# Optimization experiments

Measured on AMD Instinct MI355X. Metric: run time of the kernel, lower is better.

## Reference

```python
import jax, jax.numpy as jnp
import numpy as np

# LightGCN propagation constants
N_USERS = 50000
N_ITEMS = 100000
N_NODES = N_USERS + N_ITEMS          # rows of the symmetric normalized adjacency
N_EDGES = 2400000                    # nnz of sparse adjacency (avg degree ~16)
LATENT_DIM = 64                      # config['latent_dim_rec']
N_LAYERS = 3                         # config['lightGCN_n_layers']
BATCH = 4096


def setup_inputs() -> dict:
    key = jax.random.key(0)
    ks = jax.random.split(key, 7)
    # Embedding tables, init std=0.1 as in nn.init.normal_(std=0.1)
    emb_user = 0.1 * jax.random.normal(ks[0], (N_USERS, LATENT_DIM), dtype=jnp.float32)
    emb_item = 0.1 * jax.random.normal(ks[1], (N_ITEMS, LATENT_DIM), dtype=jnp.float32)
    # Sparse normalized adjacency in COO form (fixed structure reused every layer)
    src = jax.random.randint(ks[2], (N_EDGES,), 0, N_NODES, dtype=jnp.int32)
    dst = jax.random.randint(ks[3], (N_EDGES,), 0, N_NODES, dtype=jnp.int32)
    # values ~ 1/sqrt(deg_i * deg_j) scale for avg degree 16
    vals = jax.random.uniform(ks[4], (N_EDGES,), dtype=jnp.float32) / 16.0
    users = jax.random.randint(ks[5], (BATCH,), 0, N_USERS, dtype=jnp.int32)
    items = jax.random.randint(ks[6], (BATCH,), 0, N_ITEMS, dtype=jnp.int32)
    return {"emb_user": emb_user, "emb_item": emb_item, "vals": vals,
            "src": src, "dst": dst, "users": users, "items": items}


def _spmm(vals, src, dst, x):
    # y[dst] += vals * x[src]  == torch.sparse.mm(G, x)
    return jax.ops.segment_sum(vals[:, None] * x[src], dst, num_segments=N_NODES)


def reference(emb_user, emb_item, vals, src, dst, users, items):
    # computer(): stack layer embeddings and mean-pool, fused as running sum
    all_emb = jnp.concatenate([emb_user, emb_item], axis=0)  # [N, D]
    acc = all_emb
    x = all_emb
    for _ in range(N_LAYERS):
        x = _spmm(vals, src, dst, x)
        acc = acc + x
    light_out = acc / jnp.asarray(N_LAYERS + 1, dtype=acc.dtype)
    users_emb = light_out[users]                 # [B, D]
    items_emb = light_out[N_USERS + items]       # [B, D]
    gamma = jnp.sum(users_emb * items_emb, axis=1)  # [B]
    return gamma
```

## Files before the change

kernel.cpp:

```cpp
#include <hip/hip_runtime.h>


#define N_USERS 50000
#define N_ITEMS 100000
#define N_NODES 150000
#define N_EDGES 2400000
#define DIM 64
#define BATCH 4096

#define CHUNKS 256
#define CHUNK_EDGES 9375
#define PPT 10
#define KB 256
#define NPB 586
#define ECAP 10240
#define CONVB 2344

typedef unsigned int uint;
typedef float v2f __attribute__((ext_vector_type(2)));

__device__ __forceinline__ uint pack_bf16(float a, float b) {
    uint ua = __float_as_uint(a), ub = __float_as_uint(b);
    ua = (ua + 0x7FFFu + ((ua >> 16) & 1u)) >> 16;
    ub = (ub + 0x7FFFu + ((ub >> 16) & 1u)) >> 16;
    return ua | (ub << 16);
}

__device__ __forceinline__ v2f unpack_bf16x2(uint w) {
    v2f r;
    r.x = __uint_as_float(w << 16);
    r.y = __uint_as_float(w & 0xFFFF0000u);
    return r;
}

__global__ __launch_bounds__(1024) void part_kernel(
        const int* __restrict__ src, const int* __restrict__ dstA,
        const float* __restrict__ vals, int* __restrict__ gcur,
        int2* __restrict__ coarse,
        const float* __restrict__ emb_user, const float* __restrict__ emb_item,
        uint2* __restrict__ t0) {
    int t = threadIdx.x;
    if (blockIdx.x >= CHUNKS) {
        int i = (blockIdx.x - CHUNKS) * 1024 + t;
        if (i < N_NODES * DIM / 4) {
            const int userN4 = N_USERS * DIM / 4;
            float4 v;
            if (i < userN4) v = ((const float4*)emb_user)[i];
            else            v = ((const float4*)emb_item)[i - userN4];
            t0[i] = make_uint2(pack_bf16(v.x, v.y), pack_bf16(v.z, v.w));
        }
        return;
    }
    __shared__ int h[KB];
    __shared__ int cur[KB];
    int c = blockIdx.x;
    if (t < KB) h[t] = 0;
    __syncthreads();
    int base = c * CHUNK_EDGES;
    int d_c[PPT];
#pragma unroll
    for (int u = 0; u < PPT; ++u) {
        int i = t + u * 1024;
        d_c[u] = 0;
        if (i < CHUNK_EDGES) {
            int d = dstA[base + i];
            d_c[u] = d;
            atomicAdd(&h[(int)((unsigned)d / NPB)], 1);
        }
    }
    __syncthreads();
    if (t < KB) cur[t] = atomicAdd(&gcur[t], h[t]);
    __syncthreads();
#pragma unroll
    for (int u = 0; u < PPT; ++u) {
        int i = t + u * 1024;
        if (i < CHUNK_EDGES) {
            int e = base + i;
            int d = d_c[u];
            int b = (int)((unsigned)d / NPB);
            int dl = d - b * NPB;
            int p = atomicAdd(&cur[b], 1);
            if (p < ECAP)
                coarse[b * ECAP + p] = make_int2(src[e] | (dl << 18),
                                                 __float_as_int(vals[e]));
        }
    }
}

__global__ __launch_bounds__(1024) void p4f_fine(int2* __restrict__ coarse,
                                                 const int* __restrict__ gcur,
                                                 uint* __restrict__ rowinfo) {
    __shared__ int2 eds[ECAP];
    __shared__ int cnt[640];
    __shared__ int rs_[640];
    __shared__ int cur_[640];
    __shared__ int wsum[16];
    int k = blockIdx.x, t = threadIdx.x;
    int rbase = k * ECAP;
    int ne = min(gcur[k], ECAP);
    for (int i = t; i < ne; i += 1024) eds[i] = coarse[rbase + i];
    if (t < 640) cnt[t] = 0;
    __syncthreads();
    for (int i = t; i < ne; i += 1024)
        atomicAdd(&cnt[eds[i].x >> 18], 1);
    __syncthreads();
    int wid = t >> 6, lane = t & 63;
    if (t < 640) {
        int v = cnt[t];
        int incl = v;
#pragma unroll
        for (int o = 1; o < 64; o <<= 1) {
            int add = __shfl_up(incl, o, 64);
            if (lane >= o) incl += add;
        }
        rs_[t] = incl - v;
        if (lane == 63) wsum[wid] = incl;
    }
    __syncthreads();
    if (t < 64) {
        int vv = (lane < 10) ? wsum[lane] : 0;
        int inc2 = vv;
#pragma unroll
        for (int o = 1; o < 16; o <<= 1) {
            int add = __shfl_up(inc2, o, 64);
            if (lane >= o) inc2 += add;
        }
        if (lane < 10) wsum[lane] = inc2 - vv;
    }
    __syncthreads();
    if (t < 640) rs_[t] += wsum[wid];
    __syncthreads();
    int nodes0 = k * NPB;
    int nb = min(NPB, N_NODES - nodes0);
    if (t < nb)
        rowinfo[nodes0 + t] = (uint)(rbase + rs_[t]) | ((uint)cnt[t] << 22);
    if (t < 640) cur_[t] = rs_[t];
    __syncthreads();
    for (int i = t; i < ne; i += 1024) {
        int2 ev = eds[i];
        int dl = ev.x >> 18;
        int p = atomicAdd(&cur_[dl], 1);
        coarse[rbase + p] = make_int2(ev.x & 0x3FFFF, ev.y);
    }
}

__global__ __launch_bounds__(256) void spmm_kernel(
        const uint* __restrict__ rowinfo, const int2* __restrict__ epair,
        const uint* __restrict__ xin, uint* __restrict__ xout) {
    int n = (blockIdx.x * 256 + threadIdx.x) >> 6;
    int lane = threadIdx.x & 63;
    int g = lane >> 3;
    int l = lane & 7;
    uint ri = rowinfo[n];
    int s = (int)(ri & 0x3FFFFFu);
    int e = s + (int)(ri >> 22);
    v2f a0 = {0.f, 0.f}, a1 = {0.f, 0.f}, a2 = {0.f, 0.f}, a3 = {0.f, 0.f};
    for (int j0 = s + g; j0 < e; j0 += 16) {
        int j1 = j0 + 8;
        bool p1 = j1 < e;
        int2 ev0 = epair[j0];
        int2 ev1 = epair[p1 ? j1 : j0];
        float v0 = __int_as_float(ev0.y);
        float v1 = p1 ? __int_as_float(ev1.y) : 0.f;
        uint4 r0 = ((const uint4*)(xin + (size_t)ev0.x * 32))[l];
        uint4 r1 = ((const uint4*)(xin + (size_t)ev1.x * 32))[l];
        a0 += v0 * unpack_bf16x2(r0.x);
        a1 += v0 * unpack_bf16x2(r0.y);
        a2 += v0 * unpack_bf16x2(r0.z);
        a3 += v0 * unpack_bf16x2(r0.w);
        a0 += v1 * unpack_bf16x2(r1.x);
        a1 += v1 * unpack_bf16x2(r1.y);
        a2 += v1 * unpack_bf16x2(r1.z);
        a3 += v1 * unpack_bf16x2(r1.w);
    }
#pragma unroll
    for (int off = 8; off < 64; off <<= 1) {
        a0.x += __shfl_xor(a0.x, off, 64);
        a0.y += __shfl_xor(a0.y, off, 64);
        a1.x += __shfl_xor(a1.x, off, 64);
        a1.y += __shfl_xor(a1.y, off, 64);
        a2.x += __shfl_xor(a2.x, off, 64);
        a2.y += __shfl_xor(a2.y, off, 64);
        a3.x += __shfl_xor(a3.x, off, 64);
        a3.y += __shfl_xor(a3.y, off, 64);
    }
    if (g == 0) {
        uint4 o;
        o.x = pack_bf16(a0.x, a0.y);
        o.y = pack_bf16(a1.x, a1.y);
        o.z = pack_bf16(a2.x, a2.y);
        o.w = pack_bf16(a3.x, a3.y);
        ((uint4*)(xout + (size_t)n * 32))[l] = o;
    }
}

__global__ __launch_bounds__(256) void batch_row_kernel(
        const int* __restrict__ users, const int* __restrict__ items,
        const float* __restrict__ emb_user, const float* __restrict__ emb_item,
        const uint* __restrict__ x1, const uint* __restrict__ x2,
        const uint* __restrict__ rowinfo, const int2* __restrict__ epair,
        float4* __restrict__ rows) {
    int w = (blockIdx.x * 256 + threadIdx.x) >> 6;
    int lane = threadIdx.x & 63;
    int g = lane >> 4;
    int l = lane & 15;
    bool isU = w < BATCH;
    int b = isU ? w : w - BATCH;
    int idx = isU ? users[b] : items[b];
    int n = isU ? idx : N_USERS + idx;
    uint ri = rowinfo[n];
    int s = (int)(ri & 0x3FFFFFu);
    int e = s + (int)(ri >> 22);
    v2f a0 = {0.f, 0.f}, a1 = {0.f, 0.f};
    for (int j0 = s + g; j0 < e; j0 += 16) {
        int2 ev[4];
        float vv[4];
        uint2 rr[4];
#pragma unroll
        for (int u = 0; u < 4; ++u) {
            int j = j0 + 4 * u;
            bool p = (u == 0) || (j < e);
            ev[u] = epair[p ? j : j0];
            vv[u] = p ? __int_as_float(ev[u].y) : 0.f;
        }
#pragma unroll
        for (int u = 0; u < 4; ++u)
            rr[u] = ((const uint2*)(x2 + (size_t)ev[u].x * 32))[l];
#pragma unroll
        for (int u = 0; u < 4; ++u) {
            a0 += vv[u] * unpack_bf16x2(rr[u].x);
            a1 += vv[u] * unpack_bf16x2(rr[u].y);
        }
    }
#pragma unroll
    for (int off = 16; off < 64; off <<= 1) {
        a0.x += __shfl_xor(a0.x, off, 64);
        a0.y += __shfl_xor(a0.y, off, 64);
        a1.x += __shfl_xor(a1.x, off, 64);
        a1.y += __shfl_xor(a1.y, off, 64);
    }
    if (g == 0) {
        const float* t0row = isU ? (emb_user + (size_t)idx * DIM)
                                 : (emb_item + (size_t)idx * DIM);
        float4 x0 = ((const float4*)t0row)[l];
        uint2 w1 = ((const uint2*)(x1 + (size_t)n * 32))[l];
        uint2 w2 = ((const uint2*)(x2 + (size_t)n * 32))[l];
        v2f b10 = unpack_bf16x2(w1.x), b11 = unpack_bf16x2(w1.y);
        v2f b20 = unpack_bf16x2(w2.x), b21 = unpack_bf16x2(w2.y);
        float4 r;
        r.x = x0.x + b10.x + b20.x + a0.x;
        r.y = x0.y + b10.y + b20.y + a0.y;
        r.z = x0.z + b11.x + b21.x + a1.x;
        r.w = x0.w + b11.y + b21.y + a1.y;
        rows[(size_t)w * 16 + l] = r;
    }
}

__global__ __launch_bounds__(256) void dot_kernel(const float* __restrict__ rows,
                                                  float* __restrict__ out) {
    int t = blockIdx.x * 256 + threadIdx.x;
    int b = t >> 6;
    int lane = t & 63;
    float p = rows[(size_t)b * DIM + lane] * rows[(size_t)(BATCH + b) * DIM + lane];
#pragma unroll
    for (int o = 32; o > 0; o >>= 1) p += __shfl_down(p, o, 64);
    if (lane == 0) out[b] = p * (1.0f / 16.0f);
}

extern "C" void kernel_launch(void* const* d_in, const int* in_sizes, int n_in,
                              void* d_out, int out_size, void* d_ws, size_t ws_size,
                              hipStream_t stream) {
    const float* emb_user = (const float*)d_in[0];
    const float* emb_item = (const float*)d_in[1];
    const float* vals     = (const float*)d_in[2];
    const int*   src      = (const int*)d_in[3];
    const int*   dst      = (const int*)d_in[4];
    const int*   users    = (const int*)d_in[5];
    const int*   items    = (const int*)d_in[6];
    float* out = (float*)d_out;

    char* ws = (char*)d_ws;
    size_t off = 0;
    auto walloc = [&](size_t bytes) -> void* {
        void* p = ws + off;
        off += (bytes + 255) & ~(size_t)255;
        return p;
    };
    const size_t ROWB = (size_t)N_NODES * DIM * 2;
    uint* t0          = (uint*)walloc(ROWB);
    uint* x1          = (uint*)walloc(ROWB);
    uint* x2          = (uint*)walloc(ROWB);
    int2* coarse      = (int2*)walloc((size_t)KB * ECAP * 8);
    int*  gcur        = (int*) walloc((size_t)KB * 4);
    uint* rowinfo     = (uint*)walloc((size_t)N_NODES * 4);
    float4* rows      = (float4*)walloc((size_t)2 * BATCH * DIM * 4);

    hipMemsetAsync(gcur, 0, (size_t)KB * 4, stream);

    part_kernel<<<CHUNKS + CONVB, 1024, 0, stream>>>(
        src, dst, vals, gcur, coarse, emb_user, emb_item, (uint2*)t0);
    p4f_fine<<<KB, 1024, 0, stream>>>(coarse, gcur, rowinfo);

    spmm_kernel<<<N_NODES / 4, 256, 0, stream>>>(rowinfo, coarse, t0, x1);
    spmm_kernel<<<N_NODES / 4, 256, 0, stream>>>(rowinfo, coarse, x1, x2);
    batch_row_kernel<<<(2 * BATCH) / 4, 256, 0, stream>>>(
        users, items, emb_user, emb_item, x1, x2, rowinfo, coarse, rows);
    dot_kernel<<<(BATCH * 64) / 256, 256, 0, stream>>>((const float*)rows, out);
}
```

Before: 268.6 us.

## Map one SpMM row per 8-lane group instead of one per wavefront

```diff
diff --git a/kernel.cpp b/kernel.cpp
--- a/kernel.cpp
+++ b/kernel.cpp
@@ -147,19 +147,21 @@
 __global__ __launch_bounds__(256) void spmm_kernel(
         const uint* __restrict__ rowinfo, const int2* __restrict__ epair,
         const uint* __restrict__ xin, uint* __restrict__ xout) {
-    int n = (blockIdx.x * 256 + threadIdx.x) >> 6;
+    int wave = (blockIdx.x * 256 + threadIdx.x) >> 6;
     int lane = threadIdx.x & 63;
     int g = lane >> 3;
     int l = lane & 7;
-    uint ri = rowinfo[n];
+    int n = wave * 8 + g;
+    bool live = n < N_NODES;
+    uint ri = live ? rowinfo[n] : 0u;
     int s = (int)(ri & 0x3FFFFFu);
-    int e = s + (int)(ri >> 22);
+    int e = live ? s + (int)(ri >> 22) : s;
     v2f a0 = {0.f, 0.f}, a1 = {0.f, 0.f}, a2 = {0.f, 0.f}, a3 = {0.f, 0.f};
-    for (int j0 = s + g; j0 < e; j0 += 16) {
-        int j1 = j0 + 8;
+    for (int j = s; j < e; j += 2) {
+        int j1 = j + 1;
         bool p1 = j1 < e;
-        int2 ev0 = epair[j0];
-        int2 ev1 = epair[p1 ? j1 : j0];
+        int2 ev0 = epair[j];
+        int2 ev1 = epair[p1 ? j1 : j];
         float v0 = __int_as_float(ev0.y);
         float v1 = p1 ? __int_as_float(ev1.y) : 0.f;
         uint4 r0 = ((const uint4*)(xin + (size_t)ev0.x * 32))[l];
@@ -173,18 +175,7 @@
         a2 += v1 * unpack_bf16x2(r1.z);
         a3 += v1 * unpack_bf16x2(r1.w);
     }
-#pragma unroll
-    for (int off = 8; off < 64; off <<= 1) {
-        a0.x += __shfl_xor(a0.x, off, 64);
-        a0.y += __shfl_xor(a0.y, off, 64);
-        a1.x += __shfl_xor(a1.x, off, 64);
-        a1.y += __shfl_xor(a1.y, off, 64);
-        a2.x += __shfl_xor(a2.x, off, 64);
-        a2.y += __shfl_xor(a2.y, off, 64);
-        a3.x += __shfl_xor(a3.x, off, 64);
-        a3.y += __shfl_xor(a3.y, off, 64);
-    }
-    if (g == 0) {
+    if (live) {
         uint4 o;
         o.x = pack_bf16(a0.x, a0.y);
         o.y = pack_bf16(a1.x, a1.y);
@@ -301,8 +292,9 @@
         src, dst, vals, gcur, coarse, emb_user, emb_item, (uint2*)t0);
     p4f_fine<<<KB, 1024, 0, stream>>>(coarse, gcur, rowinfo);
 
-    spmm_kernel<<<N_NODES / 4, 256, 0, stream>>>(rowinfo, coarse, t0, x1);
-    spmm_kernel<<<N_NODES / 4, 256, 0, stream>>>(rowinfo, coarse, x1, x2);
+    const int SPMM_BLOCKS = (N_NODES / 8 * 64 + 255) / 256;
+    spmm_kernel<<<SPMM_BLOCKS, 256, 0, stream>>>(rowinfo, coarse, t0, x1);
+    spmm_kernel<<<SPMM_BLOCKS, 256, 0, stream>>>(rowinfo, coarse, x1, x2);
     batch_row_kernel<<<(2 * BATCH) / 4, 256, 0, stream>>>(
         users, items, emb_user, emb_item, x1, x2, rowinfo, coarse, rows);
     dot_kernel<<<(BATCH * 64) / 256, 256, 0, stream>>>((const float*)rows, out);
```

New measurement: 259.9 us. -3.2%, faster.
